# Kernel optimization log

Measured on AMD Instinct MI355X. Metric: run time of the kernel, lower is better.

## Reference

```python
import jax, jax.numpy as jnp
import numpy as np

B, T, P, H, LAT = 64, 256, 128, 512, 128


def _run_lstm(x, Wih, Whh, b, h0, c0):
    """Single unidirectional LSTM layer, PyTorch gate order (i,f,g,o).
    x: (B,T,in) -> outputs (B,T,H), final h (B,H)."""
    xW = jnp.einsum('bti,gi->btg', x, Wih) + b  # precompute input projection (B,T,4H)

    def step(carry, xw_t):
        h, c = carry
        g = xw_t + h @ Whh.T
        i, f, gg, o = jnp.split(g, 4, axis=-1)
        c = jax.nn.sigmoid(f) * c + jax.nn.sigmoid(i) * jnp.tanh(gg)
        h = jax.nn.sigmoid(o) * jnp.tanh(c)
        return (h, c), h

    (hT, cT), hs = jax.lax.scan(step, (h0, c0), jnp.swapaxes(xW, 0, 1))
    return jnp.swapaxes(hs, 0, 1), hT


def setup_inputs() -> dict:
    key = jax.random.key(0)
    ks = iter(jax.random.split(key, 40))
    rn = lambda shape, s=0.05: jax.random.normal(next(ks), shape, jnp.float32) * s
    inp = {
        'x': (jax.random.uniform(next(ks), (B, T, P)) < 0.1).astype(jnp.float32),
        'e0f_Wih': rn((4 * H, P)), 'e0f_Whh': rn((4 * H, H)), 'e0f_b': jnp.zeros((4 * H,), jnp.float32),
        'e0b_Wih': rn((4 * H, P)), 'e0b_Whh': rn((4 * H, H)), 'e0b_b': jnp.zeros((4 * H,), jnp.float32),
        'e1f_Wih': rn((4 * H, 2 * H)), 'e1f_Whh': rn((4 * H, H)), 'e1f_b': jnp.zeros((4 * H,), jnp.float32),
        'e1b_Wih': rn((4 * H, 2 * H)), 'e1b_Whh': rn((4 * H, H)), 'e1b_b': jnp.zeros((4 * H,), jnp.float32),
        'enc_fc_W': rn((LAT, 2 * H)), 'enc_fc_b': jnp.zeros((LAT,), jnp.float32),
        'dec_fc_W': rn((H, LAT)), 'dec_fc_b': jnp.zeros((H,), jnp.float32),
        'start_token': rn((1, 1, P), 0.1),
        'd0_Wih': rn((4 * H, P)), 'd0_Whh': rn((4 * H, H)), 'd0_b': jnp.zeros((4 * H,), jnp.float32),
        'd1_Wih': rn((4 * H, H)), 'd1_Whh': rn((4 * H, H)), 'd1_b': jnp.zeros((4 * H,), jnp.float32),
        'out_W': rn((P, H)), 'out_b': jnp.zeros((P,), jnp.float32),
        'teacher_forcing_ratio': 1,
    }
    return inp


def reference(x, e0f_Wih, e0f_Whh, e0f_b, e0b_Wih, e0b_Whh, e0b_b,
              e1f_Wih, e1f_Whh, e1f_b, e1b_Wih, e1b_Whh, e1b_b,
              enc_fc_W, enc_fc_b, dec_fc_W, dec_fc_b, start_token,
              d0_Wih, d0_Whh, d0_b, d1_Wih, d1_Whh, d1_b, out_W, out_b,
              teacher_forcing_ratio):
    b = x.shape[0]
    z0 = jnp.zeros((b, H), x.dtype)
    # ---- encoder: 2-layer bidirectional LSTM ----
    f0, _ = _run_lstm(x, e0f_Wih, e0f_Whh, e0f_b, z0, z0)
    r0, _ = _run_lstm(x[:, ::-1], e0b_Wih, e0b_Whh, e0b_b, z0, z0)
    l0 = jnp.concatenate([f0, r0[:, ::-1]], axis=-1)  # (B,T,2H)
    _, h_fwd = _run_lstm(l0, e1f_Wih, e1f_Whh, e1f_b, z0, z0)
    _, h_bwd = _run_lstm(l0[:, ::-1], e1b_Wih, e1b_Whh, e1b_b, z0, z0)
    z = jnp.concatenate([h_fwd, h_bwd], axis=-1) @ enc_fc_W.T + enc_fc_b  # (B,LAT)
    # ---- decoder: teacher-forced 2-layer LSTM ----
    h0d = z @ dec_fc_W.T + dec_fc_b  # (B,H), repeated for every layer
    xs = jnp.concatenate([jnp.broadcast_to(start_token, (b, 1, P)), x[:, :-1]], axis=1)
    o0, _ = _run_lstm(xs, d0_Wih, d0_Whh, d0_b, h0d, z0)
    o1, _ = _run_lstm(o0, d1_Wih, d1_Whh, d1_b, h0d, z0)
    x_hat = jax.nn.sigmoid(o1 @ out_W.T + out_b)  # (B,T,P)
    return x_hat, z
```

## Files before the change

kernel.cpp:

```cpp
#include <hip/hip_runtime.h>
#include <stdint.h>


typedef unsigned short u16;
typedef unsigned int u32;
typedef float f32x4 __attribute__((ext_vector_type(4)));
typedef __bf16 bf16x8 __attribute__((ext_vector_type(8)));
typedef unsigned int u32x4 __attribute__((ext_vector_type(4)));

#define AT_LD(p) __hip_atomic_load((p), __ATOMIC_RELAXED, __HIP_MEMORY_SCOPE_AGENT)
#define AT_ST(p, v) __hip_atomic_store((p), (v), __ATOMIC_RELAXED, __HIP_MEMORY_SCOPE_AGENT)

__device__ __forceinline__ u16 f2bf(float f) {
  u32 u = __builtin_bit_cast(u32, f);
  u += 0x7FFFu + ((u >> 16) & 1u);
  return (u16)(u >> 16);
}
__device__ __forceinline__ float bf2f(u16 h) {
  return __builtin_bit_cast(float, (u32)h << 16);
}
__device__ __forceinline__ bf16x8 ld8(const u16* p) {
  u32x4 v = *(const u32x4*)p;
  return __builtin_bit_cast(bf16x8, v);
}
__device__ __forceinline__ float sigf(float x) { return 1.f / (1.f + __expf(-x)); }
__device__ __forceinline__ float tanhx(float x) {
  x = fminf(fmaxf(x, -15.f), 15.f);
  float e = __expf(2.f * x);
  return (e - 1.f) / (e + 1.f);
}

__global__ void k_prep_x(const float* __restrict__ x, const float* __restrict__ st,
                         u16* __restrict__ Ax, u16* __restrict__ Axs, int n) {
  int i = blockIdx.x * 256 + threadIdx.x;
  if (i >= n) return;
  Ax[i] = f2bf(x[i]);
  int col = i & 127;
  int t = (i >> 7) & 255;
  float v = (t == 0) ? st[col] : x[i - 128];
  Axs[i] = f2bf(v);
}

struct CvtJobs {
  const float* src[13];
  u16* dst[13];
  int off[14];
};
__global__ void k_cvt_all(CvtJobs j, int total) {
  int i = blockIdx.x * 256 + threadIdx.x;
  if (i >= total) return;
  int a = 0;
#pragma unroll
  for (int k = 1; k < 13; ++k) a += (i >= j.off[k]) ? 1 : 0;
  int local = i - j.off[a];
  j.dst[a][local] = f2bf(j.src[a][local]);
}

__global__ __launch_bounds__(256) void k_gemm_bt(
    const u16* __restrict__ A, const u16* __restrict__ B, const float* __restrict__ bias,
    u16* __restrict__ Cb, float* __restrict__ Cf, int M, int N, int K, int sig) {
  __shared__ __align__(16) u16 As[128 * 64];
  __shared__ __align__(16) u16 Bs[128 * 64];
  const int m0 = blockIdx.x * 128, n0 = blockIdx.y * 128;
  const int tid = threadIdx.x, lane = tid & 63, wave = tid >> 6;
  const int wm = wave >> 1, wn = wave & 1;

  f32x4 acc[4][4];
#pragma unroll
  for (int i = 0; i < 4; ++i)
#pragma unroll
    for (int j = 0; j < 4; ++j) acc[i][j] = (f32x4){0.f, 0.f, 0.f, 0.f};

  const int nkt = K >> 6;
  for (int kt = 0; kt < nkt; ++kt) {
#pragma unroll
    for (int i = 0; i < 4; ++i) {
      int ch = tid + (i << 8);
      int row = ch >> 3, k8 = ch & 7;
      int dst = row * 128 + ((k8 * 16) ^ ((row & 7) << 4));
      u32x4 va = *(const u32x4*)(A + (size_t)(m0 + row) * K + kt * 64 + k8 * 8);
      *(u32x4*)((char*)As + dst) = va;
      u32x4 vb = *(const u32x4*)(B + (size_t)(n0 + row) * K + kt * 64 + k8 * 8);
      *(u32x4*)((char*)Bs + dst) = vb;
    }
    __syncthreads();
#pragma unroll
    for (int kk = 0; kk < 2; ++kk) {
      int kb = kk * 64 + ((lane >> 4) << 4);
      bf16x8 afr[4], bfr[4];
#pragma unroll
      for (int i = 0; i < 4; ++i) {
        int ra = wm * 64 + i * 16 + (lane & 15);
        afr[i] = ld8((const u16*)((const char*)As + ra * 128 + (kb ^ ((ra & 7) << 4))));
        int rb = wn * 64 + i * 16 + (lane & 15);
        bfr[i] = ld8((const u16*)((const char*)Bs + rb * 128 + (kb ^ ((rb & 7) << 4))));
      }
#pragma unroll
      for (int i = 0; i < 4; ++i)
#pragma unroll
        for (int j = 0; j < 4; ++j)
          acc[i][j] = __builtin_amdgcn_mfma_f32_16x16x32_bf16(afr[i], bfr[j], acc[i][j], 0, 0, 0);
    }
    __syncthreads();
  }
#pragma unroll
  for (int i = 0; i < 4; ++i) {
#pragma unroll
    for (int j = 0; j < 4; ++j) {
      int col = n0 + wn * 64 + j * 16 + (lane & 15);
      float bv = bias ? bias[col] : 0.f;
#pragma unroll
      for (int r = 0; r < 4; ++r) {
        int row = m0 + wm * 64 + i * 16 + ((lane >> 4) << 2) + r;
        float v = acc[i][j][r] + bv;
        if (sig) Cf[(size_t)row * N + col] = 1.f / (1.f + __expf(-v));
        else     Cb[(size_t)row * N + col] = f2bf(v);
      }
    }
  }
}

struct RecE {
  const u16* xW[8];
  const u16* Whh[8];
  u16* seq[8];
  float* hfin[8];
  u16* hxc[8];
  int seqstride[8]; int coloff[8]; int rev[8]; int hfinstride[8];
  int grp[8];
  u32* tags;
};

__global__ __launch_bounds__(256, 1) void k_rec_e(RecE p) {
  const int chain = blockIdx.x & 7;
  const int c = blockIdx.x >> 3;
  const int tid = threadIdx.x, lane = tid & 63, wave = tid >> 6;
  const int arow = lane & 15, kg = lane >> 4;

  const u16* __restrict__ xW = p.xW[chain];
  const u16* __restrict__ Whh = p.Whh[chain];
  u16* seq = p.seq[chain];
  float* hfin = p.hfin[chain];
  u32* hx = (u32*)p.hxc[chain];
  const int grp = p.grp[chain], rev = p.rev[chain];
  const int sstride = p.seqstride[chain], coloff = p.coloff[chain];
  const int hstride = p.hfinstride[chain];
  u32* myt = p.tags + chain * 64;

  __shared__ __align__(16) u16 Wlds[64][128][8];
  __shared__ __align__(16) u16 hbufA[8192];
  __shared__ float gbuf[4][16][32];
  __shared__ float cbuf[512];

  for (int e = tid; e < 8192; e += 256) {
    int n = e >> 6, k8 = e & 63;
    int grow = ((n >> 5) << 9) + (c << 5) + (n & 31);
    *(u32x4*)(&Wlds[k8][n][0]) = *(const u32x4*)(Whh + (size_t)grow * 512 + k8 * 8);
  }
  for (int e = tid; e < 512; e += 256) cbuf[e] = 0.f;
  for (int e = tid; e < 4096; e += 256) AT_ST(hx + e, 0u);
  asm volatile("s_waitcnt vmcnt(0)" ::: "memory");
  __syncthreads();
  if (tid == 0) AT_ST(myt + c, 1u);

  for (int t = 0; t < 256; ++t) {
    const int t_eff = rev ? 255 - t : t;
    const int slot = t & 3;
    const int slotn = (t + 1) & 3;

    float xwv[4][2];
#pragma unroll
    for (int r4 = 0; r4 < 4; ++r4) {
      int row = (kg << 2) + r4;
      const u16* xwp = xW + (((size_t)((grp * 16 + row) * 256 + t_eff)) << 11) +
                       (wave << 9) + (c << 5);
      xwv[r4][0] = bf2f(xwp[arow]);
      xwv[r4][1] = bf2f(xwp[arow + 16]);
    }
    if (wave == 0) {
      u32 thr = (u32)(t + 1);
      while (true) {
        int ok = 1;
        if (lane < 16 && lane != c) ok = (AT_LD(myt + lane) >= thr);
        if (__all(ok)) break;
        __builtin_amdgcn_s_sleep(1);
      }
    }
    __syncthreads();
    __builtin_amdgcn_sched_barrier(0);

#pragma unroll
    for (int i = 0; i < 4; ++i) {
      int cid = tid + (i << 8);
      int row = cid >> 6, ch8 = cid & 63;
      const u32* src = hx + slot * 4096 + row * 256 + ch8 * 4;
      u32x4 v;
      v.x = AT_LD(src + 0); v.y = AT_LD(src + 1);
      v.z = AT_LD(src + 2); v.w = AT_LD(src + 3);
      *(u32x4*)((char*)hbufA + row * 1024 + ((ch8 << 4) ^ ((row & 7) << 4))) = v;
    }
    __syncthreads();

    bf16x8 af[16];
#pragma unroll
    for (int kt = 0; kt < 16; ++kt)
      af[kt] = ld8((const u16*)((const char*)hbufA + arow * 1024 +
                                ((kt * 64 + (kg << 4)) ^ ((arow & 7) << 4))));
    f32x4 acc0 = {0.f, 0.f, 0.f, 0.f};
    f32x4 acc1 = {0.f, 0.f, 0.f, 0.f};
#pragma unroll
    for (int kt = 0; kt < 16; ++kt) {
      const u16* bp = &Wlds[(kt << 2) + kg][(wave << 5) + arow][0];
      bf16x8 b0 = ld8(bp);
      bf16x8 b1 = ld8(bp + 128);
      acc0 = __builtin_amdgcn_mfma_f32_16x16x32_bf16(af[kt], b0, acc0, 0, 0, 0);
      acc1 = __builtin_amdgcn_mfma_f32_16x16x32_bf16(af[kt], b1, acc1, 0, 0, 0);
    }
#pragma unroll
    for (int r4 = 0; r4 < 4; ++r4) {
      gbuf[wave][(kg << 2) + r4][arow] = acc0[r4] + xwv[r4][0];
      gbuf[wave][(kg << 2) + r4][arow + 16] = acc1[r4] + xwv[r4][1];
    }
    __syncthreads();

    u32 pk0 = 0, pk1 = 0; int row2 = 0, j0 = 0;
    float hhv[4] = {0.f, 0.f, 0.f, 0.f};
    if (tid >= 128) {
      int t2 = tid - 128;
      row2 = t2 >> 3; int q = t2 & 7; j0 = q << 2;
#pragma unroll
      for (int jj = 0; jj < 4; ++jj) {
        int col = j0 + jj;
        float iv = gbuf[0][row2][col];
        float fv = gbuf[1][row2][col];
        float gv = gbuf[2][row2][col];
        float ov = gbuf[3][row2][col];
        int ci = (row2 << 5) + col;
        float cc = sigf(fv) * cbuf[ci] + sigf(iv) * tanhx(gv);
        cbuf[ci] = cc;
        hhv[jj] = sigf(ov) * tanhx(cc);
      }
      pk0 = (u32)f2bf(hhv[0]) | ((u32)f2bf(hhv[1]) << 16);
      pk1 = (u32)f2bf(hhv[2]) | ((u32)f2bf(hhv[3]) << 16);
      u32* dst = hx + slotn * 4096 + row2 * 256 + (c << 4) + (q << 1);
      AT_ST(dst, pk0);
      AT_ST(dst + 1, pk1);
      asm volatile("s_waitcnt vmcnt(0)" ::: "memory");
    }
    __syncthreads();
    if (tid == 128) AT_ST(myt + c, (u32)(t + 2));
    if (tid >= 128) {
      if (seq) {
        u32* sp = (u32*)(seq + ((size_t)((grp * 16 + row2) * 256 + t_eff)) * sstride +
                         coloff + (c << 5) + j0);
        sp[0] = pk0; sp[1] = pk1;
      }
      if (hfin && t == 255) {
        float* hp = hfin + (size_t)(grp * 16 + row2) * hstride + (c << 5) + j0;
        hp[0] = hhv[0]; hp[1] = hhv[1]; hp[2] = hhv[2]; hp[3] = hhv[3];
      }
    }
  }
}

struct Rec2 {
  const u16* xW[8];
  const u16* Whh[8];
  const u16* Wih[8];
  const float* bias[8];
  const float* h0[8];
  u16* seq[8];
  float* hfin[8];
  u16* hxc[8];
  int prod[8];
  int seqstride[8]; int coloff[8]; int rev[8]; int hfinstride[8];
  int grp[8]; int fused[8]; int fullp[8];
  u32* tags;
};

__global__ __launch_bounds__(256, 1) void k_rec2(Rec2 p) {
  const int chain = blockIdx.x & 7;
  const int c = blockIdx.x >> 3;
  const int tid = threadIdx.x, lane = tid & 63, wave = tid >> 6;
  const int arow = lane & 15, kg = lane >> 4;

  const u16* __restrict__ xW = p.xW[chain];
  const u16* __restrict__ Whh = p.Whh[chain];
  const u16* __restrict__ Wih = p.Wih[chain];
  const float* __restrict__ bias = p.bias[chain];
  const float* __restrict__ h0 = p.h0[chain];
  u16* seq = p.seq[chain];
  float* hfin = p.hfin[chain];
  u32* hx = (u32*)p.hxc[chain];
  const u32* hxp = (const u32*)p.hxc[p.prod[chain]];
  const int grp = p.grp[chain], rev = p.rev[chain];
  const int fused = p.fused[chain], fullp = p.fullp[chain];
  const int sstride = p.seqstride[chain], coloff = p.coloff[chain];
  const int hstride = p.hfinstride[chain];
  u32* myt = p.tags + chain * 64;
  const u32* pt = p.tags + p.prod[chain] * 64;

  __shared__ __align__(16) u16 Wlds[64][64][8];
  __shared__ __align__(16) u16 Xlds[64][64][8];
  __shared__ __align__(16) u16 hbufA[8192];
  __shared__ float gbuf[4][16][16];
  __shared__ float cbuf[256];
  __shared__ float bbuf[64];

  for (int e = tid; e < 4096; e += 256) {
    int n = e >> 6, k8 = e & 63;
    int grow = ((n >> 4) << 9) + (c << 4) + (n & 15);
    *(u32x4*)(&Wlds[k8][n][0]) = *(const u32x4*)(Whh + (size_t)grow * 512 + k8 * 8);
    if (fused)
      *(u32x4*)(&Xlds[k8][n][0]) = *(const u32x4*)(Wih + (size_t)grow * 512 + k8 * 8);
  }
  if (tid < 64) bbuf[tid] = fused ? bias[((tid >> 4) << 9) + (c << 4) + (tid & 15)] : 0.f;
  cbuf[tid] = 0.f;
  if (tid < 128) {
    int row = tid >> 3, q = tid & 7;
    float a = 0.f, b2 = 0.f;
    if (h0) {
      a = h0[(size_t)(grp * 16 + row) * 512 + (c << 4) + 2 * q];
      b2 = h0[(size_t)(grp * 16 + row) * 512 + (c << 4) + 2 * q + 1];
    }
    u32 pk = (u32)f2bf(a) | ((u32)f2bf(b2) << 16);
    AT_ST(hx + (size_t)c * 128 + (row << 3) + q, pk);
  }
  asm volatile("s_waitcnt vmcnt(0)" ::: "memory");
  __syncthreads();
  if (tid == 0) AT_ST(myt + c, 1u);

  for (int t = 0; t < 256; ++t) {
    const int t_eff = rev ? 255 - t : t;
    const int slot = fullp ? t : (t & 3);
    const int slotn = fullp ? (t + 1) : ((t + 1) & 3);

    float xwv[4] = {0.f, 0.f, 0.f, 0.f};
    if (!fused) {
#pragma unroll
      for (int r4 = 0; r4 < 4; ++r4) {
        int row = (kg << 2) + r4;
        xwv[r4] = bf2f(xW[(((size_t)((grp * 16 + row) * 256 + t_eff)) << 11) +
                          (wave << 9) + (c << 4) + arow]);
      }
    }
    if (wave == 0) {
      u32 thr_own = (u32)(t + 1), thr_prod = (u32)(t + 2);
      while (true) {
        int ok = 1;
        if (lane < 32) {
          if (lane != c) ok = (AT_LD(myt + lane) >= thr_own);
        } else if (fused) {
          ok = (AT_LD(pt + (lane - 32)) >= thr_prod);
        }
        if (__all(ok)) break;
        __builtin_amdgcn_s_sleep(1);
      }
    }
    __syncthreads();
    __builtin_amdgcn_sched_barrier(0);

#pragma unroll
    for (int i = 0; i < 4; ++i) {
      int cid = tid + (i << 8);
      int row = cid >> 6, ch8 = cid & 63;
      const u32* src = hx + ((size_t)slot * 32 + (ch8 >> 1)) * 128 +
                       (row << 3) + ((ch8 & 1) << 2);
      u32x4 v;
      v.x = AT_LD(src + 0); v.y = AT_LD(src + 1);
      v.z = AT_LD(src + 2); v.w = AT_LD(src + 3);
      *(u32x4*)((char*)hbufA + row * 1024 + ((ch8 << 4) ^ ((row & 7) << 4))) = v;
    }
    bf16x8 xf[16];
    if (fused) {
#pragma unroll
      for (int kt = 0; kt < 16; ++kt) {
        const u32* hp = hxp + ((size_t)(t + 1) * 32 + 2 * kt + (kg >> 1)) * 128 +
                        (arow << 3) + ((kg & 1) << 2);
        u32x4 v;
        v.x = AT_LD(hp + 0); v.y = AT_LD(hp + 1);
        v.z = AT_LD(hp + 2); v.w = AT_LD(hp + 3);
        xf[kt] = __builtin_bit_cast(bf16x8, v);
      }
    }
    __syncthreads();

    bf16x8 af[16];
#pragma unroll
    for (int kt = 0; kt < 16; ++kt)
      af[kt] = ld8((const u16*)((const char*)hbufA + arow * 1024 +
                                ((kt * 64 + (kg << 4)) ^ ((arow & 7) << 4))));
    f32x4 ae = {0.f, 0.f, 0.f, 0.f}, ao = {0.f, 0.f, 0.f, 0.f};
#pragma unroll
    for (int kt = 0; kt < 16; ++kt) {
      bf16x8 bw = ld8(&Wlds[(kt << 2) + kg][(wave << 4) + arow][0]);
      if (kt & 1) ao = __builtin_amdgcn_mfma_f32_16x16x32_bf16(af[kt], bw, ao, 0, 0, 0);
      else        ae = __builtin_amdgcn_mfma_f32_16x16x32_bf16(af[kt], bw, ae, 0, 0, 0);
      if (fused) {
        bf16x8 bx = ld8(&Xlds[(kt << 2) + kg][(wave << 4) + arow][0]);
        if (kt & 1) ae = __builtin_amdgcn_mfma_f32_16x16x32_bf16(xf[kt], bx, ae, 0, 0, 0);
        else        ao = __builtin_amdgcn_mfma_f32_16x16x32_bf16(xf[kt], bx, ao, 0, 0, 0);
      }
    }
#pragma unroll
    for (int r4 = 0; r4 < 4; ++r4)
      gbuf[wave][(kg << 2) + r4][arow] = ae[r4] + ao[r4] + xwv[r4];
    __syncthreads();

    u32 pk = 0; int row2 = 0, j0 = 0;
    float hh0 = 0.f, hh1 = 0.f;
    if (tid >= 128) {
      int t2 = tid - 128;
      row2 = t2 >> 3; int q = t2 & 7; j0 = q << 1;
      float i0 = gbuf[0][row2][j0], i1 = gbuf[0][row2][j0 + 1];
      float f0 = gbuf[1][row2][j0], f1 = gbuf[1][row2][j0 + 1];
      float g0 = gbuf[2][row2][j0], g1 = gbuf[2][row2][j0 + 1];
      float o0v = gbuf[3][row2][j0], o1v = gbuf[3][row2][j0 + 1];
      if (fused) {
        i0 += bbuf[j0]; i1 += bbuf[j0 + 1];
        f0 += bbuf[16 + j0]; f1 += bbuf[16 + j0 + 1];
        g0 += bbuf[32 + j0]; g1 += bbuf[32 + j0 + 1];
        o0v += bbuf[48 + j0]; o1v += bbuf[48 + j0 + 1];
      }
      int ci = (row2 << 4) + j0;
      float cc0 = sigf(f0) * cbuf[ci] + sigf(i0) * tanhx(g0);
      float cc1 = sigf(f1) * cbuf[ci + 1] + sigf(i1) * tanhx(g1);
      cbuf[ci] = cc0; cbuf[ci + 1] = cc1;
      hh0 = sigf(o0v) * tanhx(cc0);
      hh1 = sigf(o1v) * tanhx(cc1);
      pk = (u32)f2bf(hh0) | ((u32)f2bf(hh1) << 16);
      AT_ST(hx + ((size_t)slotn * 32 + c) * 128 + (row2 << 3) + q, pk);
      asm volatile("s_waitcnt vmcnt(0)" ::: "memory");
    }
    __syncthreads();
    if (tid == 128) AT_ST(myt + c, (u32)(t + 2));
    if (tid >= 128) {
      if (seq)
        *(u32*)(seq + ((size_t)((grp * 16 + row2) * 256 + t_eff)) * sstride +
                coloff + (c << 4) + j0) = pk;
      if (hfin && t == 255) {
        hfin[(size_t)(grp * 16 + row2) * hstride + (c << 4) + j0] = hh0;
        hfin[(size_t)(grp * 16 + row2) * hstride + (c << 4) + j0 + 1] = hh1;
      }
    }
  }
}

__global__ void k_enc_head(const float* __restrict__ hcat, const float* __restrict__ W,
                           const float* __restrict__ b, float* __restrict__ zws,
                           float* __restrict__ zout) {
  int bi = blockIdx.x, j = threadIdx.x;
  const float* h = hcat + bi * 1024;
  const float* w = W + j * 1024;
  float s = b[j];
  for (int k = 0; k < 1024; ++k) s += h[k] * w[k];
  zws[bi * 128 + j] = s;
  zout[bi * 128 + j] = s;
}

__global__ void k_dec_head(const float* __restrict__ z, const float* __restrict__ W,
                           const float* __restrict__ b, float* __restrict__ h0d) {
  int bi = blockIdx.x, j = threadIdx.x;
  const float* zz = z + bi * 128;
  const float* w = W + j * 128;
  float s = b[j];
  for (int k = 0; k < 128; ++k) s += zz[k] * w[k];
  h0d[bi * 512 + j] = s;
}

extern "C" void kernel_launch(void* const* d_in, const int* in_sizes, int n_in,
                              void* d_out, int out_size, void* d_ws, size_t ws_size,
                              hipStream_t stream) {
  (void)in_sizes; (void)n_in; (void)out_size;
  const float* x        = (const float*)d_in[0];
  const float* e0f_Wih  = (const float*)d_in[1];
  const float* e0f_Whh  = (const float*)d_in[2];
  const float* e0f_b    = (const float*)d_in[3];
  const float* e0b_Wih  = (const float*)d_in[4];
  const float* e0b_Whh  = (const float*)d_in[5];
  const float* e0b_b    = (const float*)d_in[6];
  const float* e1f_Wih  = (const float*)d_in[7];
  const float* e1f_Whh  = (const float*)d_in[8];
  const float* e1f_b    = (const float*)d_in[9];
  const float* e1b_Wih  = (const float*)d_in[10];
  const float* e1b_Whh  = (const float*)d_in[11];
  const float* e1b_b    = (const float*)d_in[12];
  const float* enc_fc_W = (const float*)d_in[13];
  const float* enc_fc_b = (const float*)d_in[14];
  const float* dec_fc_W = (const float*)d_in[15];
  const float* dec_fc_b = (const float*)d_in[16];
  const float* start_tk = (const float*)d_in[17];
  const float* d0_Wih   = (const float*)d_in[18];
  const float* d0_Whh   = (const float*)d_in[19];
  const float* d0_b     = (const float*)d_in[20];
  const float* d1_Wih   = (const float*)d_in[21];
  const float* d1_Whh   = (const float*)d_in[22];
  const float* d1_b     = (const float*)d_in[23];
  const float* out_W    = (const float*)d_in[24];
  const float* out_b    = (const float*)d_in[25];

  uintptr_t base = (uintptr_t)d_ws;
  size_t off = 0;
  auto carve = [&](size_t bytes) -> void* {
    off = (off + 255) & ~(size_t)255;
    void* p = (void*)(base + off);
    off += bytes;
    return p;
  };
  u16* Ax     = (u16*)carve((size_t)2097152 * 2);
  u16* Axs    = (u16*)carve((size_t)2097152 * 2);
  u16* Wb_e0f = (u16*)carve((size_t)262144 * 2);
  u16* Wb_e0b = (u16*)carve((size_t)262144 * 2);
  u16* Wb_d0  = (u16*)carve((size_t)262144 * 2);
  u16* Wb_e1f = (u16*)carve((size_t)2097152 * 2);
  u16* Wb_e1b = (u16*)carve((size_t)2097152 * 2);
  u16* Wb_d1  = (u16*)carve((size_t)1048576 * 2);
  u16* Wb_out = (u16*)carve((size_t)65536 * 2);
  u16* Wh_e0f = (u16*)carve((size_t)1048576 * 2);
  u16* Wh_e0b = (u16*)carve((size_t)1048576 * 2);
  u16* Wh_e1f = (u16*)carve((size_t)1048576 * 2);
  u16* Wh_e1b = (u16*)carve((size_t)1048576 * 2);
  u16* Wh_d0  = (u16*)carve((size_t)1048576 * 2);
  u16* Wh_d1  = (u16*)carve((size_t)1048576 * 2);
  u16* slot0  = (u16*)carve((size_t)16384 * 2048 * 2);
  u16* slot1  = (u16*)carve((size_t)16384 * 2048 * 2);
  u16* l0     = (u16*)carve((size_t)33619968);
  u16* hxring = (u16*)carve((size_t)524288);
  float* hcat = (float*)carve((size_t)65536 * 4);
  float* zws  = (float*)carve((size_t)8192 * 4);
  float* h0d  = (float*)carve((size_t)32768 * 4);
  u32* tags0  = (u32*)carve(2048);
  u32* tags1  = (u32*)carve(2048);
  u32* tags2  = (u32*)carve(2048);
  if (off > ws_size) return;

  u16* o1     = l0;
  u16* hxprod = l0 + 8388608;

  (void)hipMemsetAsync(tags0, 0, 6144, stream);

  k_prep_x<<<8192, 256, 0, stream>>>(x, start_tk, Ax, Axs, 2097152);
  {
    CvtJobs j{};
    const float* s[13] = {e0f_Wih, e0b_Wih, d0_Wih, e1f_Wih, e1b_Wih, d1_Wih, out_W,
                          e0f_Whh, e0b_Whh, e1f_Whh, e1b_Whh, d0_Whh, d1_Whh};
    u16* d[13] = {Wb_e0f, Wb_e0b, Wb_d0, Wb_e1f, Wb_e1b, Wb_d1, Wb_out,
                  Wh_e0f, Wh_e0b, Wh_e1f, Wh_e1b, Wh_d0, Wh_d1};
    int n[13] = {262144, 262144, 262144, 2097152, 2097152, 1048576, 65536,
                 1048576, 1048576, 1048576, 1048576, 1048576, 1048576};
    int acc = 0;
    for (int k = 0; k < 13; ++k) { j.src[k] = s[k]; j.dst[k] = d[k]; j.off[k] = acc; acc += n[k]; }
    j.off[13] = acc;
    k_cvt_all<<<(acc + 255) / 256, 256, 0, stream>>>(j, acc);
  }

  k_gemm_bt<<<dim3(128, 16), 256, 0, stream>>>(Ax, Wb_e0f, e0f_b, slot0, nullptr, 16384, 2048, 128, 0);
  k_gemm_bt<<<dim3(128, 16), 256, 0, stream>>>(Ax, Wb_e0b, e0b_b, slot1, nullptr, 16384, 2048, 128, 0);
  {
    RecE r{};
    for (int ch = 0; ch < 8; ++ch) {
      int dir2 = ch >> 2, g = ch & 3;
      r.xW[ch] = dir2 ? slot1 : slot0;
      r.Whh[ch] = dir2 ? Wh_e0b : Wh_e0f;
      r.seq[ch] = l0; r.seqstride[ch] = 1024; r.coloff[ch] = dir2 ? 512 : 0;
      r.rev[ch] = dir2; r.hfin[ch] = nullptr; r.hfinstride[ch] = 0;
      r.grp[ch] = g;
      r.hxc[ch] = hxring + (size_t)ch * 32768;
    }
    r.tags = tags0;
    k_rec_e<<<128, 256, 0, stream>>>(r);
  }
  k_gemm_bt<<<dim3(128, 16), 256, 0, stream>>>(l0, Wb_e1f, e1f_b, slot0, nullptr, 16384, 2048, 1024, 0);
  k_gemm_bt<<<dim3(128, 16), 256, 0, stream>>>(l0, Wb_e1b, e1b_b, slot1, nullptr, 16384, 2048, 1024, 0);
  {
    RecE r{};
    for (int ch = 0; ch < 8; ++ch) {
      int dir2 = ch >> 2, g = ch & 3;
      r.xW[ch] = dir2 ? slot1 : slot0;
      r.Whh[ch] = dir2 ? Wh_e1b : Wh_e1f;
      r.seq[ch] = nullptr; r.seqstride[ch] = 0; r.coloff[ch] = 0;
      r.rev[ch] = dir2; r.hfin[ch] = hcat + (dir2 ? 512 : 0); r.hfinstride[ch] = 1024;
      r.grp[ch] = g;
      r.hxc[ch] = hxring + (size_t)ch * 32768;
    }
    r.tags = tags1;
    k_rec_e<<<128, 256, 0, stream>>>(r);
  }
  k_enc_head<<<64, 128, 0, stream>>>(hcat, enc_fc_W, enc_fc_b, zws, ((float*)d_out) + 2097152);
  k_dec_head<<<64, 512, 0, stream>>>(zws, dec_fc_W, dec_fc_b, h0d);
  k_gemm_bt<<<dim3(128, 16), 256, 0, stream>>>(Axs, Wb_d0, d0_b, slot0, nullptr, 16384, 2048, 128, 0);
  {
    Rec2 r{};
    for (int ch = 0; ch < 4; ++ch) {
      r.xW[ch] = slot0;
      r.Whh[ch] = Wh_d0;
      r.Wih[ch] = nullptr; r.bias[ch] = nullptr; r.h0[ch] = h0d;
      r.seq[ch] = nullptr; r.seqstride[ch] = 0; r.coloff[ch] = 0;
      r.rev[ch] = 0; r.hfin[ch] = nullptr; r.hfinstride[ch] = 0;
      r.grp[ch] = ch; r.fused[ch] = 0; r.fullp[ch] = 1; r.prod[ch] = 0;
      r.hxc[ch] = hxprod + (size_t)ch * 2105344;
    }
    for (int ch = 4; ch < 8; ++ch) {
      r.xW[ch] = nullptr;
      r.Whh[ch] = Wh_d1;
      r.Wih[ch] = Wb_d1; r.bias[ch] = d1_b; r.h0[ch] = h0d;
      r.seq[ch] = o1; r.seqstride[ch] = 512; r.coloff[ch] = 0;
      r.rev[ch] = 0; r.hfin[ch] = nullptr; r.hfinstride[ch] = 0;
      r.grp[ch] = ch - 4; r.fused[ch] = 1; r.fullp[ch] = 0; r.prod[ch] = ch - 4;
      r.hxc[ch] = hxring + (size_t)ch * 32768;
    }
    r.tags = tags2;
    k_rec2<<<256, 256, 0, stream>>>(r);
  }
  k_gemm_bt<<<dim3(128, 1), 256, 0, stream>>>(o1, Wb_out, out_b, nullptr, (float*)d_out, 16384, 128, 512, 1);
}
```

Baseline: 5.147 ms.

## Publish per-wave step flags and drop barrier before progress signal

```diff
diff --git a/kernel.cpp b/kernel.cpp
--- a/kernel.cpp
+++ b/kernel.cpp
@@ -161,7 +161,7 @@
   for (int e = tid; e < 4096; e += 256) AT_ST(hx + e, 0u);
   asm volatile("s_waitcnt vmcnt(0)" ::: "memory");
   __syncthreads();
-  if (tid == 0) AT_ST(myt + c, 1u);
+  if (tid == 0) { AT_ST(myt + c * 2, 1u); AT_ST(myt + c * 2 + 1, 1u); }
 
   for (int t = 0; t < 256; ++t) {
     const int t_eff = rev ? 255 - t : t;
@@ -181,7 +181,7 @@
       u32 thr = (u32)(t + 1);
       while (true) {
         int ok = 1;
-        if (lane < 16 && lane != c) ok = (AT_LD(myt + lane) >= thr);
+        if (lane < 32) ok = (AT_LD(myt + lane) >= thr);
         if (__all(ok)) break;
         __builtin_amdgcn_s_sleep(1);
       }
@@ -223,11 +223,10 @@
     }
     __syncthreads();
 
-    u32 pk0 = 0, pk1 = 0; int row2 = 0, j0 = 0;
-    float hhv[4] = {0.f, 0.f, 0.f, 0.f};
     if (tid >= 128) {
       int t2 = tid - 128;
-      row2 = t2 >> 3; int q = t2 & 7; j0 = q << 2;
+      int row2 = t2 >> 3; int q = t2 & 7; int j0 = q << 2;
+      float hhv[4];
 #pragma unroll
       for (int jj = 0; jj < 4; ++jj) {
         int col = j0 + jj;
@@ -240,16 +239,13 @@
         cbuf[ci] = cc;
         hhv[jj] = sigf(ov) * tanhx(cc);
       }
-      pk0 = (u32)f2bf(hhv[0]) | ((u32)f2bf(hhv[1]) << 16);
-      pk1 = (u32)f2bf(hhv[2]) | ((u32)f2bf(hhv[3]) << 16);
+      u32 pk0 = (u32)f2bf(hhv[0]) | ((u32)f2bf(hhv[1]) << 16);
+      u32 pk1 = (u32)f2bf(hhv[2]) | ((u32)f2bf(hhv[3]) << 16);
       u32* dst = hx + slotn * 4096 + row2 * 256 + (c << 4) + (q << 1);
       AT_ST(dst, pk0);
       AT_ST(dst + 1, pk1);
       asm volatile("s_waitcnt vmcnt(0)" ::: "memory");
-    }
-    __syncthreads();
-    if (tid == 128) AT_ST(myt + c, (u32)(t + 2));
-    if (tid >= 128) {
+      if (lane == 0) AT_ST(myt + c * 2 + (wave - 2), (u32)(t + 2));
       if (seq) {
         u32* sp = (u32*)(seq + ((size_t)((grp * 16 + row2) * 256 + t_eff)) * sstride +
                          coloff + (c << 5) + j0);
@@ -328,7 +324,7 @@
   }
   asm volatile("s_waitcnt vmcnt(0)" ::: "memory");
   __syncthreads();
-  if (tid == 0) AT_ST(myt + c, 1u);
+  if (tid == 0) { AT_ST(myt + c * 2, 1u); AT_ST(myt + c * 2 + 1, 1u); }
 
   for (int t = 0; t < 256; ++t) {
     const int t_eff = rev ? 255 - t : t;
@@ -345,14 +341,16 @@
       }
     }
     if (wave == 0) {
-      u32 thr_own = (u32)(t + 1), thr_prod = (u32)(t + 2);
+      u32 thr_own = (u32)(t + 1);
       while (true) {
-        int ok = 1;
-        if (lane < 32) {
-          if (lane != c) ok = (AT_LD(myt + lane) >= thr_own);
-        } else if (fused) {
-          ok = (AT_LD(pt + (lane - 32)) >= thr_prod);
-        }
+        int ok = (AT_LD(myt + lane) >= thr_own);
+        if (__all(ok)) break;
+        __builtin_amdgcn_s_sleep(1);
+      }
+    } else if (wave == 1 && fused) {
+      u32 thr_prod = (u32)(t + 2);
+      while (true) {
+        int ok = (AT_LD(pt + lane) >= thr_prod);
         if (__all(ok)) break;
         __builtin_amdgcn_s_sleep(1);
       }
@@ -407,11 +405,9 @@
       gbuf[wave][(kg << 2) + r4][arow] = ae[r4] + ao[r4] + xwv[r4];
     __syncthreads();
 
-    u32 pk = 0; int row2 = 0, j0 = 0;
-    float hh0 = 0.f, hh1 = 0.f;
     if (tid >= 128) {
       int t2 = tid - 128;
-      row2 = t2 >> 3; int q = t2 & 7; j0 = q << 1;
+      int row2 = t2 >> 3; int q = t2 & 7; int j0 = q << 1;
       float i0 = gbuf[0][row2][j0], i1 = gbuf[0][row2][j0 + 1];
       float f0 = gbuf[1][row2][j0], f1 = gbuf[1][row2][j0 + 1];
       float g0 = gbuf[2][row2][j0], g1 = gbuf[2][row2][j0 + 1];
@@ -426,15 +422,12 @@
       float cc0 = sigf(f0) * cbuf[ci] + sigf(i0) * tanhx(g0);
       float cc1 = sigf(f1) * cbuf[ci + 1] + sigf(i1) * tanhx(g1);
       cbuf[ci] = cc0; cbuf[ci + 1] = cc1;
-      hh0 = sigf(o0v) * tanhx(cc0);
-      hh1 = sigf(o1v) * tanhx(cc1);
-      pk = (u32)f2bf(hh0) | ((u32)f2bf(hh1) << 16);
+      float hh0 = sigf(o0v) * tanhx(cc0);
+      float hh1 = sigf(o1v) * tanhx(cc1);
+      u32 pk = (u32)f2bf(hh0) | ((u32)f2bf(hh1) << 16);
       AT_ST(hx + ((size_t)slotn * 32 + c) * 128 + (row2 << 3) + q, pk);
       asm volatile("s_waitcnt vmcnt(0)" ::: "memory");
-    }
-    __syncthreads();
-    if (tid == 128) AT_ST(myt + c, (u32)(t + 2));
-    if (tid >= 128) {
+      if (lane == 0) AT_ST(myt + c * 2 + (wave - 2), (u32)(t + 2));
       if (seq)
         *(u32*)(seq + ((size_t)((grp * 16 + row2) * 256 + t_eff)) * sstride +
                 coloff + (c << 4) + j0) = pk;
```

After: 5.637 ms. 1.1x slower.
